# Performance work log

Measured on AMD Instinct MI355X. Metric: run time of the kernel, lower is better.

The kernel has to match this reference:

```python
import jax, jax.numpy as jnp
import numpy as np

HID, KQ, V = 1024, 64, 64
B, S = 8, 2048
NEG_INF = -1000000000.0


def setup_inputs() -> dict:
    key = jax.random.key(0)
    ks = jax.random.split(key, 10)
    return {
        "k_hidden_inputs": jax.random.normal(ks[0], (B, S, HID), jnp.float32),
        "q_hidden_inputs": jax.random.normal(ks[1], (B, S, HID), jnp.float32),
        "v_hidden_inputs": jax.random.normal(ks[2], (B, S, HID), jnp.float32),
        "mask": jax.random.randint(ks[3], (B, S, S), 0, 2, jnp.int32),
        "Wq": jax.random.normal(ks[4], (HID, KQ), jnp.float32) * 0.02,
        "bq": jnp.zeros((KQ,), jnp.float32),
        "Wk": jax.random.normal(ks[5], (HID, KQ), jnp.float32) * 0.02,
        "bk": jnp.zeros((KQ,), jnp.float32),
        "Wv": jax.random.normal(ks[6], (HID, V), jnp.float32) * 0.02,
        "bv": jnp.zeros((V,), jnp.float32),
    }


def reference(k_hidden_inputs, q_hidden_inputs, v_hidden_inputs, mask,
              Wq, bq, Wk, bk, Wv, bv):
    keys = jnp.einsum('bsh,hd->bsd', k_hidden_inputs, Wk) + bk
    queries = jnp.einsum('bsh,hd->bsd', q_hidden_inputs, Wq) + bq
    values = jnp.einsum('bsh,hd->bsd', v_hidden_inputs, Wv) + bv
    # scaled dot-product scores: [B, S_q, S_k]
    scores = jnp.einsum('bqd,bkd->bqk', queries, keys) / jnp.sqrt(jnp.float32(KQ))
    scores = jnp.where(mask == 0, jnp.float32(NEG_INF), scores)
    attn = jax.nn.softmax(scores, axis=-1)
    return jnp.einsum('bqk,bkv->bqv', attn, values)
```

## Files before the change

### kernel.cpp

```cpp
#include <hip/hip_runtime.h>

#define HIDDEN 1024
#define NB 8
#define SEQ 2048
#define DH 64

typedef long long i64;
typedef unsigned short u16;
typedef __attribute__((ext_vector_type(8))) _Float16 half8;
typedef __attribute__((ext_vector_type(4))) float f32x4;

#define MFMA16F __builtin_amdgcn_mfma_f32_16x16x32_f16

__device__ __forceinline__ u16 f2h(float x) {
    _Float16 h = (_Float16)x;
    return __builtin_bit_cast(u16, h);
}
__device__ __forceinline__ void gl_lds16(const void* g, void* l) {
    __builtin_amdgcn_global_load_lds(
        (const __attribute__((address_space(1))) unsigned int*)g,
        (__attribute__((address_space(3))) unsigned int*)l, 16, 0, 0);
}

__global__ __launch_bounds__(256) void wimg_prep8(
    const float* __restrict__ Wq, const float* __restrict__ Wk, const float* __restrict__ Wv,
    u16* __restrict__ Wimg)
{
    const int t = blockIdx.x * 256 + threadIdx.x;
    const int te = t >> 13;
    const int rem = t & 8191;
    const int p = rem >> 10;
    const int rem2 = rem & 1023;
    const int n = rem2 >> 4;
    const int pos = rem2 & 15;
    const float* W = te == 0 ? Wq : te == 1 ? Wk : Wv;
    const int g = pos ^ (n & 7);
    const int k0 = p * 128 + g * 8;
    u16* dst = Wimg + (i64)t * 8;
    #pragma unroll
    for (int j = 0; j < 8; ++j)
        dst[j] = f2h(W[(i64)(k0 + j) * DH + n]);
}

__global__ __launch_bounds__(256) void proj_mfma8(
    const float* __restrict__ qh, const float* __restrict__ kh, const float* __restrict__ vh,
    const u16* __restrict__ Wimg,
    const float* __restrict__ bq, const float* __restrict__ bk, const float* __restrict__ bv,
    u16* __restrict__ Qb, u16* __restrict__ Kb, u16* __restrict__ Vt)
{
    const int te = blockIdx.y;
    const float* A    = te == 0 ? qh : te == 1 ? kh : vh;
    const float* bias = te == 0 ? bq : te == 1 ? bk : bv;
    const int row0 = blockIdx.x << 5;
    const int t = threadIdx.x;
    const int w = t >> 6, lane = t & 63;
    const int lr = lane & 15, lg = lane >> 4;
    const int wr = (w & 1) << 4;
    const int wc = (w >> 1) << 5;

    __shared__ __attribute__((aligned(16))) float AL[2][32 * 128];
    __shared__ __attribute__((aligned(16))) u16  WL[2][64 * 128];

    const u16* Wte = Wimg + (i64)te * 8 * 8192;

    const float* asrc[4]; int adst[4];
    #pragma unroll
    for (int i = 0; i < 4; ++i) {
        const int r0 = 8 * w + 2 * i;
        const int rl = r0 + (lane >> 5);
        asrc[i] = A + (i64)(row0 + rl) * HIDDEN + (((lane & 31) ^ (rl & 7)) << 2);
        adst[i] = r0 * 128;
    }
    const u16* wsrc[4]; int wdst[4];
    #pragma unroll
    for (int i = 0; i < 4; ++i) {
        const int n0 = 16 * w + 4 * i;
        wsrc[i] = Wte + n0 * 128 + (lane << 3);
        wdst[i] = n0 * 128;
    }

    f32x4 acc[2] = {};

#define STAGE8(bufi, p) { \
        _Pragma("unroll") \
        for (int i_ = 0; i_ < 4; ++i_) \
            gl_lds16(asrc[i_] + (p) * 128, &AL[bufi][adst[i_]]); \
        _Pragma("unroll") \
        for (int i_ = 0; i_ < 4; ++i_) \
            gl_lds16(wsrc[i_] + (p) * 8192, &WL[bufi][wdst[i_]]); }

    STAGE8(0, 0)

    int buf = 0;
    #pragma unroll 1
    for (int p = 0; p < 8; ++p) {
        asm volatile("s_waitcnt vmcnt(0)" ::: "memory");
        __syncthreads();
        if (p < 7) STAGE8(buf ^ 1, p + 1)
        const int x = lr & 7;
        #pragma unroll
        for (int ks = 0; ks < 4; ++ks) {
            const int b0 = ks * 8 + lg * 2;
            const float4 fa = *(const float4*)&AL[buf][(wr + lr) * 128 + ((b0 ^ x) << 2)];
            const float4 fb = *(const float4*)&AL[buf][(wr + lr) * 128 + (((b0 + 1) ^ x) << 2)];
            half8 a;
            a[0] = (_Float16)fa.x; a[1] = (_Float16)fa.y;
            a[2] = (_Float16)fa.z; a[3] = (_Float16)fa.w;
            a[4] = (_Float16)fb.x; a[5] = (_Float16)fb.y;
            a[6] = (_Float16)fb.z; a[7] = (_Float16)fb.w;
            #pragma unroll
            for (int nt = 0; nt < 2; ++nt) {
                const int n = wc + nt * 16 + lr;
                const int pos = (ks * 4 + lg) ^ x;
                const half8 bfr = *(const half8*)&WL[buf][n * 128 + (pos << 3)];
                acc[nt] = MFMA16F(a, bfr, acc[nt], 0, 0, 0);
            }
        }
        buf ^= 1;
    }
#undef STAGE8

    #pragma unroll
    for (int nt = 0; nt < 2; ++nt) {
        const int col = wc + nt * 16 + lr;
        const float bb = bias[col];
        #pragma unroll
        for (int r = 0; r < 4; ++r) {
            const i64 grow = row0 + wr + (lg << 2) + r;
            const u16 v = f2h(acc[nt][r] + bb);
            if (te == 0)      Qb[grow * DH + col] = v;
            else if (te == 1) Kb[grow * DH + col] = v;
            else {
                const i64 bb2 = grow >> 11, key = grow & 2047;
                Vt[(bb2 * DH + col) * SEQ + key] = v;
            }
        }
    }
}

__global__ __launch_bounds__(64) void attn_mfma(
    const u16* __restrict__ Qb, const u16* __restrict__ Kb, const u16* __restrict__ Vt,
    const int* __restrict__ mask, float* __restrict__ out)
{
    __shared__ __attribute__((aligned(16))) u16 Kl[2][64 * 64];
    __shared__ __attribute__((aligned(16))) u16 Vl[2][64 * 64];
    __shared__ __attribute__((aligned(16))) u16 Pl[16][72];

    const int lane = threadIdx.x;
    const int lr = lane & 15, lg = lane >> 4;
    const int b  = blockIdx.x >> 7;
    const int q0 = (blockIdx.x & 127) << 4;

    const i64 qrow = (i64)b * SEQ + q0 + lr;
    const half8 qf0 = *(const half8*)(Qb + qrow * DH + lg * 8);
    const half8 qf1 = *(const half8*)(Qb + qrow * DH + 32 + lg * 8);

    const int srow = lane >> 3;
    const int scb  = lane & 7;

    f32x4 oacc[4] = {};
    float rs0 = 0.f, rs1 = 0.f, rs2 = 0.f, rs3 = 0.f;

    {
        const i64 kbase = (i64)b * SEQ;
        #pragma unroll
        for (int i = 0; i < 8; ++i) {
            int row = i * 8 + srow, cb = scb ^ (row & 7);
            gl_lds16(Kb + (kbase + row) * DH + cb * 8, &Kl[0][i * 512]);
        }
        #pragma unroll
        for (int i = 0; i < 8; ++i) {
            int row = i * 8 + srow, cb = scb ^ (row & 7);
            gl_lds16(Vt + ((i64)b * DH + row) * SEQ + cb * 8, &Vl[0][i * 512]);
        }
    }

    #pragma unroll 1
    for (int t = 0; t < 32; ++t) {
        const int kt = t * 64;
        const int buf = t & 1;

        int mv[16];
        #pragma unroll
        for (int tt = 0; tt < 4; ++tt)
            #pragma unroll
            for (int r = 0; r < 4; ++r)
                mv[tt * 4 + r] =
                    mask[((i64)b * SEQ + q0 + lg * 4 + r) * SEQ + kt + tt * 16 + lr];

        if (t < 31) {
            const int kn = kt + 64;
            const i64 kbase = (i64)b * SEQ + kn;
            #pragma unroll
            for (int i = 0; i < 8; ++i) {
                int row = i * 8 + srow, cb = scb ^ (row & 7);
                gl_lds16(Kb + (kbase + row) * DH + cb * 8, &Kl[buf ^ 1][i * 512]);
            }
            #pragma unroll
            for (int i = 0; i < 8; ++i) {
                int row = i * 8 + srow, cb = scb ^ (row & 7);
                gl_lds16(Vt + ((i64)b * DH + row) * SEQ + kn + cb * 8, &Vl[buf ^ 1][i * 512]);
            }
            asm volatile("s_waitcnt vmcnt(32)" ::: "memory");
        } else {
            asm volatile("s_waitcnt vmcnt(16)" ::: "memory");
        }

        f32x4 sacc[4] = {};
        #pragma unroll
        for (int tt = 0; tt < 4; ++tt) {
            int row = tt * 16 + lr, x = row & 7;
            half8 k0 = *(const half8*)&Kl[buf][row * 64 + ((lg) ^ x) * 8];
            half8 k1 = *(const half8*)&Kl[buf][row * 64 + ((lg + 4) ^ x) * 8];
            sacc[tt] = MFMA16F(qf0, k0, sacc[tt], 0, 0, 0);
            sacc[tt] = MFMA16F(qf1, k1, sacc[tt], 0, 0, 0);
        }

        #pragma unroll
        for (int tt = 0; tt < 4; ++tt) {
            #pragma unroll
            for (int r = 0; r < 4; ++r) {
                float p = (mv[tt * 4 + r] != 0) ? __expf(sacc[tt][r] * 0.125f) : 0.0f;
                if      (r == 0) rs0 += p;
                else if (r == 1) rs1 += p;
                else if (r == 2) rs2 += p;
                else             rs3 += p;
                Pl[lg * 4 + r][tt * 16 + lr] = f2h(p);
            }
        }

        const half8 p0 = *(const half8*)&Pl[lr][lg * 8];
        const half8 p1 = *(const half8*)&Pl[lr][32 + lg * 8];
        #pragma unroll
        for (int vt = 0; vt < 4; ++vt) {
            int row = vt * 16 + lr, x = row & 7;
            half8 v0 = *(const half8*)&Vl[buf][row * 64 + ((lg) ^ x) * 8];
            half8 v1 = *(const half8*)&Vl[buf][row * 64 + ((lg + 4) ^ x) * 8];
            oacc[vt] = MFMA16F(p0, v0, oacc[vt], 0, 0, 0);
            oacc[vt] = MFMA16F(p1, v1, oacc[vt], 0, 0, 0);
        }
    }

    float rs[4] = {rs0, rs1, rs2, rs3};
    #pragma unroll
    for (int r = 0; r < 4; ++r) {
        float v = rs[r];
        v += __shfl_xor(v, 1, 64);
        v += __shfl_xor(v, 2, 64);
        v += __shfl_xor(v, 4, 64);
        v += __shfl_xor(v, 8, 64);
        rs[r] = 1.0f / v;
    }
    #pragma unroll
    for (int vt = 0; vt < 4; ++vt)
        #pragma unroll
        for (int r = 0; r < 4; ++r)
            out[((i64)b * SEQ + q0 + lg * 4 + r) * DH + vt * 16 + lr] = oacc[vt][r] * rs[r];
}

extern "C" void kernel_launch(void* const* d_in, const int* in_sizes, int n_in,
                              void* d_out, int out_size, void* d_ws, size_t ws_size,
                              hipStream_t stream) {
    const float* kh   = (const float*)d_in[0];
    const float* qh   = (const float*)d_in[1];
    const float* vh   = (const float*)d_in[2];
    const int*   mask = (const int*)  d_in[3];
    const float* Wq   = (const float*)d_in[4];
    const float* bq   = (const float*)d_in[5];
    const float* Wk   = (const float*)d_in[6];
    const float* bk   = (const float*)d_in[7];
    const float* Wv   = (const float*)d_in[8];
    const float* bv   = (const float*)d_in[9];
    float* out = (float*)d_out;

    u16* Wimg = (u16*)d_ws;
    u16* Qb   = Wimg + 3 * 8 * 8192;
    u16* Kb   = Qb + (i64)NB * SEQ * DH;
    u16* Vt   = Kb + (i64)NB * SEQ * DH;

    wimg_prep8<<<96, 256, 0, stream>>>(Wq, Wk, Wv, Wimg);
    proj_mfma8<<<dim3(512, 3), 256, 0, stream>>>(qh, kh, vh, Wimg,
                                                 bq, bk, bv, Qb, Kb, Vt);
    attn_mfma<<<1024, 64, 0, stream>>>(Qb, Kb, Vt, mask, out);
}
```

Measured before the change: 115.0 us.

## Restructure projection GEMM into single-wave blocks with deeper async K pipeline

The projection kernel now runs one 64-thread wave per block. Each block handles 16 rows across all 64 output columns, in 16 K-steps of 64 instead of 8 steps of 128. Because only one wave touches LDS, the block barrier is dropped, and a partial vmcnt wait lets the next stage's global-to-LDS loads overlap the current MFMAs. The weight image is re-laid out to match the new 64-wide K slices. The trade-off is that each block re-reads the full weight image, so total weight traffic through L2 doubles. In return the kernel gets more independent blocks and fewer synchronisation stalls.

```diff
diff --git a/kernel.cpp b/kernel.cpp
--- a/kernel.cpp
+++ b/kernel.cpp
@@ -22,27 +22,27 @@
         (__attribute__((address_space(3))) unsigned int*)l, 16, 0, 0);
 }
 
-__global__ __launch_bounds__(256) void wimg_prep8(
+__global__ __launch_bounds__(256) void wimg_prep16(
     const float* __restrict__ Wq, const float* __restrict__ Wk, const float* __restrict__ Wv,
     u16* __restrict__ Wimg)
 {
     const int t = blockIdx.x * 256 + threadIdx.x;
     const int te = t >> 13;
     const int rem = t & 8191;
-    const int p = rem >> 10;
-    const int rem2 = rem & 1023;
-    const int n = rem2 >> 4;
-    const int pos = rem2 & 15;
+    const int p = rem >> 9;
+    const int rem2 = rem & 511;
+    const int n = rem2 >> 3;
+    const int pos = rem2 & 7;
     const float* W = te == 0 ? Wq : te == 1 ? Wk : Wv;
     const int g = pos ^ (n & 7);
-    const int k0 = p * 128 + g * 8;
+    const int k0 = p * 64 + g * 8;
     u16* dst = Wimg + (i64)t * 8;
     #pragma unroll
     for (int j = 0; j < 8; ++j)
         dst[j] = f2h(W[(i64)(k0 + j) * DH + n]);
 }
 
-__global__ __launch_bounds__(256) void proj_mfma8(
+__global__ __launch_bounds__(64) void proj_mfma10(
     const float* __restrict__ qh, const float* __restrict__ kh, const float* __restrict__ vh,
     const u16* __restrict__ Wimg,
     const float* __restrict__ bq, const float* __restrict__ bk, const float* __restrict__ bv,
@@ -51,82 +51,73 @@
     const int te = blockIdx.y;
     const float* A    = te == 0 ? qh : te == 1 ? kh : vh;
     const float* bias = te == 0 ? bq : te == 1 ? bk : bv;
-    const int row0 = blockIdx.x << 5;
-    const int t = threadIdx.x;
-    const int w = t >> 6, lane = t & 63;
+    const int row0 = blockIdx.x << 4;
+    const int lane = threadIdx.x;
     const int lr = lane & 15, lg = lane >> 4;
-    const int wr = (w & 1) << 4;
-    const int wc = (w >> 1) << 5;
-
-    __shared__ __attribute__((aligned(16))) float AL[2][32 * 128];
-    __shared__ __attribute__((aligned(16))) u16  WL[2][64 * 128];
-
-    const u16* Wte = Wimg + (i64)te * 8 * 8192;
-
-    const float* asrc[4]; int adst[4];
+
+    __shared__ __attribute__((aligned(16))) float AL[2][1024];
+    __shared__ __attribute__((aligned(16))) u16  WL[2][4096];
+
+    const u16* Wte = Wimg + (i64)te * 16 * 4096;
+
+    const float* asrc[4];
     #pragma unroll
     for (int i = 0; i < 4; ++i) {
-        const int r0 = 8 * w + 2 * i;
-        const int rl = r0 + (lane >> 5);
-        asrc[i] = A + (i64)(row0 + rl) * HIDDEN + (((lane & 31) ^ (rl & 7)) << 2);
-        adst[i] = r0 * 128;
-    }
-    const u16* wsrc[4]; int wdst[4];
-    #pragma unroll
-    for (int i = 0; i < 4; ++i) {
-        const int n0 = 16 * w + 4 * i;
-        wsrc[i] = Wte + n0 * 128 + (lane << 3);
-        wdst[i] = n0 * 128;
-    }
-
-    f32x4 acc[2] = {};
-
-#define STAGE8(bufi, p) { \
+        const int ar = 4 * i + (lane >> 4);
+        const int ab = (lane & 15) ^ (ar & 15);
+        asrc[i] = A + (i64)(row0 + ar) * HIDDEN + (ab << 2);
+    }
+    const u16* wsrc = Wte + (lane << 3);
+
+    f32x4 acc[4] = {};
+
+#define STAGE(S, B) { \
         _Pragma("unroll") \
         for (int i_ = 0; i_ < 4; ++i_) \
-            gl_lds16(asrc[i_] + (p) * 128, &AL[bufi][adst[i_]]); \
+            gl_lds16(asrc[i_] + (S) * 64, &AL[B][i_ * 256]); \
         _Pragma("unroll") \
-        for (int i_ = 0; i_ < 4; ++i_) \
-            gl_lds16(wsrc[i_] + (p) * 8192, &WL[bufi][wdst[i_]]); }
-
-    STAGE8(0, 0)
-
-    int buf = 0;
+        for (int j_ = 0; j_ < 8; ++j_) \
+            gl_lds16(wsrc + (S) * 4096 + j_ * 512, &WL[B][j_ * 512]); }
+
+    STAGE(0, 0)
+
     #pragma unroll 1
-    for (int p = 0; p < 8; ++p) {
-        asm volatile("s_waitcnt vmcnt(0)" ::: "memory");
-        __syncthreads();
-        if (p < 7) STAGE8(buf ^ 1, p + 1)
-        const int x = lr & 7;
-        #pragma unroll
-        for (int ks = 0; ks < 4; ++ks) {
+    for (int s = 0; s < 16; ++s) {
+        const int buf = s & 1;
+        if (s < 15) {
+            STAGE(s + 1, buf ^ 1)
+            asm volatile("s_waitcnt vmcnt(12)" ::: "memory");
+        } else {
+            asm volatile("s_waitcnt vmcnt(0)" ::: "memory");
+        }
+        #pragma unroll
+        for (int ks = 0; ks < 2; ++ks) {
             const int b0 = ks * 8 + lg * 2;
-            const float4 fa = *(const float4*)&AL[buf][(wr + lr) * 128 + ((b0 ^ x) << 2)];
-            const float4 fb = *(const float4*)&AL[buf][(wr + lr) * 128 + (((b0 + 1) ^ x) << 2)];
+            const float4 fa = *(const float4*)&AL[buf][lr * 64 + ((b0 ^ lr) << 2)];
+            const float4 fb = *(const float4*)&AL[buf][lr * 64 + (((b0 + 1) ^ lr) << 2)];
             half8 a;
             a[0] = (_Float16)fa.x; a[1] = (_Float16)fa.y;
             a[2] = (_Float16)fa.z; a[3] = (_Float16)fa.w;
             a[4] = (_Float16)fb.x; a[5] = (_Float16)fb.y;
             a[6] = (_Float16)fb.z; a[7] = (_Float16)fb.w;
             #pragma unroll
-            for (int nt = 0; nt < 2; ++nt) {
-                const int n = wc + nt * 16 + lr;
-                const int pos = (ks * 4 + lg) ^ x;
-                const half8 bfr = *(const half8*)&WL[buf][n * 128 + (pos << 3)];
-                acc[nt] = MFMA16F(a, bfr, acc[nt], 0, 0, 0);
-            }
-        }
-        buf ^= 1;
-    }
-#undef STAGE8
-
-    #pragma unroll
-    for (int nt = 0; nt < 2; ++nt) {
-        const int col = wc + nt * 16 + lr;
+            for (int nt = 0; nt < 4; ++nt) {
+                const int n = nt * 16 + lr;
+                const int pos = (ks * 4 + lg) ^ (n & 7);
+                const half8 b = *(const half8*)&WL[buf][n * 64 + (pos << 3)];
+                acc[nt] = MFMA16F(a, b, acc[nt], 0, 0, 0);
+            }
+        }
+    }
+#undef STAGE
+
+    #pragma unroll
+    for (int nt = 0; nt < 4; ++nt) {
+        const int col = nt * 16 + lr;
         const float bb = bias[col];
         #pragma unroll
         for (int r = 0; r < 4; ++r) {
-            const i64 grow = row0 + wr + (lg << 2) + r;
+            const i64 grow = row0 + (lg << 2) + r;
             const u16 v = f2h(acc[nt][r] + bb);
             if (te == 0)      Qb[grow * DH + col] = v;
             else if (te == 1) Kb[grow * DH + col] = v;
@@ -274,12 +265,12 @@
     float* out = (float*)d_out;
 
     u16* Wimg = (u16*)d_ws;
-    u16* Qb   = Wimg + 3 * 8 * 8192;
+    u16* Qb   = Wimg + 3 * 16 * 4096;
     u16* Kb   = Qb + (i64)NB * SEQ * DH;
     u16* Vt   = Kb + (i64)NB * SEQ * DH;
 
-    wimg_prep8<<<96, 256, 0, stream>>>(Wq, Wk, Wv, Wimg);
-    proj_mfma8<<<dim3(512, 3), 256, 0, stream>>>(qh, kh, vh, Wimg,
-                                                 bq, bk, bv, Qb, Kb, Vt);
+    wimg_prep16<<<96, 256, 0, stream>>>(Wq, Wk, Wv, Wimg);
+    proj_mfma10<<<dim3(1024, 3), 64, 0, stream>>>(qh, kh, vh, Wimg,
+                                                  bq, bk, bv, Qb, Kb, Vt);
     attn_mfma<<<1024, 64, 0, stream>>>(Qb, Kb, Vt, mask, out);
 }
```

Result: slower. 122.5 us (+6.5%).
